# Performance work log

Hardware: AMD Instinct MI355X
Metric: run time of the kernel (lower is better)

Reference implementation:

```python
import jax, jax.numpy as jnp
import numpy as np
import math

NUM_HEADS = 32
NUM_KV_HEADS = 8
HEAD_DIM = 128
ROPE_THETA = 10000.0


def _rope_cos_sin(position_ids, head_dim, dtype):
    # inv_freq: [head_dim/2]
    inv_freq = 1.0 / (ROPE_THETA ** (jnp.arange(0, head_dim, 2, dtype=jnp.float32) / head_dim))
    # freqs: [B, S, head_dim/2]
    freqs = position_ids.astype(jnp.float32)[:, :, None] * inv_freq[None, None, :]
    emb = jnp.concatenate([freqs, freqs], axis=-1)  # [B, S, head_dim]
    return jnp.cos(emb).astype(dtype), jnp.sin(emb).astype(dtype)


def _rotate_half(x):
    h = x.shape[-1] // 2
    return jnp.concatenate([-x[..., h:], x[..., :h]], axis=-1)


def setup_inputs() -> dict:
    key = jax.random.key(0)
    ks = jax.random.split(key, 5)
    B, S, H = 1, 2048, 4096
    kv_dim = NUM_KV_HEADS * HEAD_DIM
    return {
        "hidden_states": jax.random.normal(ks[0], (B, S, H), dtype=jnp.float32),
        "position_ids": jnp.arange(S, dtype=jnp.int64 if jax.config.jax_enable_x64 else jnp.int32)[None, :].repeat(B, axis=0),
        "Wq": jax.random.normal(ks[1], (H, H), dtype=jnp.float32) * 0.02,
        "Wk": jax.random.normal(ks[2], (kv_dim, H), dtype=jnp.float32) * 0.02,
        "Wv": jax.random.normal(ks[3], (kv_dim, H), dtype=jnp.float32) * 0.02,
        "Wo": jax.random.normal(ks[4], (H, H), dtype=jnp.float32) * 0.02,
    }


def reference(hidden_states, position_ids, Wq, Wk, Wv, Wo):
    B, S, H = hidden_states.shape
    groups = NUM_HEADS // NUM_KV_HEADS

    # QKV projections (nn.Linear: x @ W.T, no bias)
    q = (hidden_states @ Wq.T).reshape(B, S, NUM_HEADS, HEAD_DIM).transpose(0, 2, 1, 3)
    k = (hidden_states @ Wk.T).reshape(B, S, NUM_KV_HEADS, HEAD_DIM).transpose(0, 2, 1, 3)
    v = (hidden_states @ Wv.T).reshape(B, S, NUM_KV_HEADS, HEAD_DIM).transpose(0, 2, 1, 3)

    # RoPE
    cos, sin = _rope_cos_sin(position_ids, HEAD_DIM, q.dtype)
    cos = cos[:, None, :, :]  # [B,1,S,hd]
    sin = sin[:, None, :, :]
    q = q * cos + _rotate_half(q) * sin
    k = k * cos + _rotate_half(k) * sin

    # repeat_kv: expand KV heads to match Q heads
    k = jnp.repeat(k, groups, axis=1)  # [B, NUM_HEADS, S, hd]
    v = jnp.repeat(v, groups, axis=1)

    # scores + causal mask + fp32 softmax
    scores = jnp.einsum("bhqd,bhkd->bhqk", q, k) / math.sqrt(HEAD_DIM)
    causal = jnp.tril(jnp.ones((S, S), dtype=bool))
    scores = jnp.where(causal[None, None, :, :], scores, jnp.finfo(jnp.float32).min)
    attn = jax.nn.softmax(scores.astype(jnp.float32), axis=-1).astype(q.dtype)

    # attention output + output projection
    out = jnp.einsum("bhqk,bhkd->bhqd", attn, v)
    out = out.transpose(0, 2, 1, 3).reshape(B, S, H)
    return out @ Wo.T
```

## Files before the change

kernel.cpp:

```cpp
#include <hip/hip_runtime.h>
#include <stdint.h>


typedef __attribute__((ext_vector_type(8))) __bf16 bf16x8;
typedef __attribute__((ext_vector_type(4))) float floatx4;

#define S_LEN 2048
#define HID   4096
#define NH    32
#define NKV   8
#define HD    128

__device__ __forceinline__ unsigned short f2bf(float f) {
  union { float f; uint32_t u; } v; v.f = f;
  return (unsigned short)((v.u + 0x7fffu + ((v.u >> 16) & 1u)) >> 16);
}

__device__ __forceinline__ void gload_lds16(const unsigned short* g, unsigned short* l) {
  __builtin_amdgcn_global_load_lds(
      (const __attribute__((address_space(1))) void*)g,
      (__attribute__((address_space(3))) void*)l,
      16, 0, 0);
}

__global__ void cast_bf16_kernel(const float* __restrict__ in,
                                 unsigned short* __restrict__ out, int n4) {
  int i = blockIdx.x * blockDim.x + threadIdx.x;
  if (i >= n4) return;
  float4 f = ((const float4*)in)[i];
  ushort4 o = make_ushort4(f2bf(f.x), f2bf(f.y), f2bf(f.z), f2bf(f.w));
  ((ushort4*)out)[i] = o;
}

#define BM 128
#define BN 128
#define BK 32

__global__ __launch_bounds__(256) void gemm_bt_kernel(
    const unsigned short* __restrict__ A,
    const unsigned short* __restrict__ B,
    float* __restrict__ C, int M, int N, int K) {
  __shared__ unsigned short As[BM * BK];
  __shared__ unsigned short Bs[BN * BK];
  const int m0 = blockIdx.y * BM;
  const int n0 = blockIdx.x * BN;
  const int tid = threadIdx.x;
  const int lane = tid & 63;
  const int l15 = lane & 15;
  const int quad = lane >> 4;
  const int w = tid >> 6;
  const int wm = (w >> 1) * 64;
  const int wn = (w & 1) * 64;

  floatx4 acc[4][4];
#pragma unroll
  for (int i = 0; i < 4; i++)
#pragma unroll
    for (int j = 0; j < 4; j++) acc[i][j] = (floatx4){0.f, 0.f, 0.f, 0.f};

  const int c0 = tid, c1 = tid + 256;
  const int r0 = c0 >> 2, o0 = (c0 & 3) * 8;
  const int r1 = c1 >> 2, o1 = (c1 & 3) * 8;

  for (int k0 = 0; k0 < K; k0 += BK) {
    __syncthreads();
    gload_lds16(A + (size_t)(m0 + r0) * K + k0 + o0, As + c0 * 8);
    gload_lds16(A + (size_t)(m0 + r1) * K + k0 + o1, As + c1 * 8);
    gload_lds16(B + (size_t)(n0 + r0) * K + k0 + o0, Bs + c0 * 8);
    gload_lds16(B + (size_t)(n0 + r1) * K + k0 + o1, Bs + c1 * 8);
    __syncthreads();

    bf16x8 a_frag[4], b_frag[4];
#pragma unroll
    for (int mt = 0; mt < 4; mt++)
      a_frag[mt] = *(const bf16x8*)&As[(wm + mt * 16 + l15) * BK + quad * 8];
#pragma unroll
    for (int nt = 0; nt < 4; nt++)
      b_frag[nt] = *(const bf16x8*)&Bs[(wn + nt * 16 + l15) * BK + quad * 8];
#pragma unroll
    for (int mt = 0; mt < 4; mt++)
#pragma unroll
      for (int nt = 0; nt < 4; nt++)
        acc[mt][nt] = __builtin_amdgcn_mfma_f32_16x16x32_bf16(
            a_frag[mt], b_frag[nt], acc[mt][nt], 0, 0, 0);
  }

#pragma unroll
  for (int mt = 0; mt < 4; mt++) {
#pragma unroll
    for (int nt = 0; nt < 4; nt++) {
      const int row = m0 + wm + mt * 16 + quad * 4;
      const int col = n0 + wn + nt * 16 + l15;
#pragma unroll
      for (int r = 0; r < 4; r++)
        C[(size_t)(row + r) * N + col] = acc[mt][nt][r];
    }
  }
}

__global__ void rope_kernel(const float* __restrict__ Cqkv,
                            const int* __restrict__ pos_ids,
                            unsigned short* __restrict__ Qb,
                            unsigned short* __restrict__ Kb) {
  int t = blockIdx.x * blockDim.x + threadIdx.x;
  int j = t & 63;
  int s = t >> 6;
  int hh = blockIdx.y;
  float pos = (float)pos_ids[s];
  float ang = pos * exp2f(-0.20762050593045222f * (float)j);
  float c = cosf(ang), sn = sinf(ang);
  if (hh < NH) {
    const float* row = Cqkv + (size_t)s * 6144 + hh * HD;
    float x1 = row[j], x2 = row[j + 64];
    unsigned short* q = Qb + ((size_t)hh * S_LEN + s) * HD;
    q[j]      = f2bf(x1 * c - x2 * sn);
    q[j + 64] = f2bf(x2 * c + x1 * sn);
  } else {
    int kh = hh - NH;
    const float* row = Cqkv + (size_t)s * 6144 + HID + kh * HD;
    float x1 = row[j], x2 = row[j + 64];
    unsigned short* k = Kb + ((size_t)kh * S_LEN + s) * HD;
    k[j]      = f2bf(x1 * c - x2 * sn);
    k[j + 64] = f2bf(x2 * c + x1 * sn);
  }
}

__global__ void vtrans_kernel(const float* __restrict__ Cqkv,
                              unsigned short* __restrict__ Vt) {
  int t = blockIdx.x * blockDim.x + threadIdx.x;
  int s = t & (S_LEN - 1);
  int d = (t >> 11) & (HD - 1);
  int kh = t >> 18;
  Vt[((size_t)kh * HD + d) * S_LEN + s] =
      f2bf(Cqkv[(size_t)s * 6144 + (HID + NKV * HD) + kh * HD + d]);
}

__global__ __launch_bounds__(256, 2) void flash_attn_kernel(
    const unsigned short* __restrict__ Qb, const unsigned short* __restrict__ Kb,
    const unsigned short* __restrict__ Vt, unsigned short* __restrict__ O) {
  __shared__ unsigned short Ks[2][64 * 128];
  __shared__ unsigned short Vs[2][128 * 64];
  __shared__ unsigned short Ps[4][2][16 * 64];
  const int qb = gridDim.x - 1 - blockIdx.x;
  const int q0 = qb * 128;
  const int h = blockIdx.y;
  const int kvh = h >> 2;
  const int tid = threadIdx.x;
  const int lane = tid & 63;
  const int w = tid >> 6;
  const int l15 = lane & 15;
  const int quad = lane >> 4;
  const int qlo = q0 + w * 32;

  const unsigned short* Qh = Qb + (size_t)h * S_LEN * HD;
  const unsigned short* Kh = Kb + (size_t)kvh * S_LEN * HD;
  const unsigned short* Vh = Vt + (size_t)kvh * HD * S_LEN;

  const int kr_[4] = {(tid) >> 4, (tid + 256) >> 4, (tid + 512) >> 4, (tid + 768) >> 4};
  const int nkt = q0 / 64 + 2;

#pragma unroll
  for (int it = 0; it < 4; it++) {
    int c = tid + it * 256;
    int kr = c >> 4, kj = (c & 15) ^ (kr & 15);
    gload_lds16(Kh + (size_t)kr * HD + kj * 8, Ks[0] + c * 8);
    int vd = c >> 3, vj = (c & 7) ^ (vd & 7);
    gload_lds16(Vh + (size_t)vd * S_LEN + vj * 8, Vs[0] + c * 8);
  }

  bf16x8 q_frag[2][4];
#pragma unroll
  for (int mf = 0; mf < 2; mf++)
#pragma unroll
    for (int kk = 0; kk < 4; kk++)
      q_frag[mf][kk] = *(const bf16x8*)&Qh[(size_t)(qlo + mf * 16 + l15) * HD + kk * 32 + quad * 8];

  bf16x8 ones_frag;
  {
    union { unsigned short u; __bf16 b; } ov;
    ov.u = (l15 == 0) ? 0x3F80 : 0;
#pragma unroll
    for (int j = 0; j < 8; j++) ones_frag[j] = ov.b;
  }

  floatx4 o_acc[2][8];
  floatx4 o_l[2];
#pragma unroll
  for (int mf = 0; mf < 2; mf++) {
#pragma unroll
    for (int i = 0; i < 8; i++) o_acc[mf][i] = (floatx4){0.f, 0.f, 0.f, 0.f};
    o_l[mf] = (floatx4){0.f, 0.f, 0.f, 0.f};
  }
  const float SC2 = 0.12751738f;

  for (int kt = 0; kt < nkt; kt++) {
    const int kbase = kt * 64;
    const int buf = kt & 1;
    __syncthreads();

    if (kt + 1 < nkt) {
      const int kb2 = kbase + 64;
#pragma unroll
      for (int it = 0; it < 4; it++) {
        int c = tid + it * 256;
        int kr = c >> 4, kj = (c & 15) ^ (kr & 15);
        gload_lds16(Kh + (size_t)(kb2 + kr) * HD + kj * 8, Ks[buf ^ 1] + c * 8);
        int vd = c >> 3, vj = (c & 7) ^ (vd & 7);
        gload_lds16(Vh + (size_t)vd * S_LEN + kb2 + vj * 8, Vs[buf ^ 1] + c * 8);
      }
    }

    if (kbase <= qlo + 31) {
      floatx4 s_acc[2][4];
#pragma unroll
      for (int mf = 0; mf < 2; mf++)
#pragma unroll
        for (int nt = 0; nt < 4; nt++) s_acc[mf][nt] = (floatx4){0.f, 0.f, 0.f, 0.f};
#pragma unroll
      for (int kk = 0; kk < 4; kk++)
#pragma unroll
        for (int nt = 0; nt < 4; nt++) {
          bf16x8 k_frag = *(const bf16x8*)&Ks[buf][(nt * 16 + l15) * 128 + (((kk * 4 + quad) ^ l15) * 8)];
#pragma unroll
          for (int mf = 0; mf < 2; mf++)
            s_acc[mf][nt] = __builtin_amdgcn_mfma_f32_16x16x32_bf16(
                q_frag[mf][kk], k_frag, s_acc[mf][nt], 0, 0, 0);
        }

      const bool diag = (kbase + 63 > qlo);
#pragma unroll
      for (int mf = 0; mf < 2; mf++) {
#pragma unroll
        for (int nt = 0; nt < 4; nt++) {
          int kc = kbase + nt * 16 + l15;
          int qrow = qlo + mf * 16 + quad * 4;
          int chunk2 = nt * 2 + (l15 >> 3);
          int coff = l15 & 7;
#pragma unroll
          for (int r = 0; r < 4; r++) {
            float pv = exp2f(s_acc[mf][nt][r] * SC2);
            if (diag && kc > qrow + r) pv = 0.f;
            int row = quad * 4 + r;
            Ps[w][mf][row * 64 + ((chunk2 ^ (row & 7)) * 8) + coff] = f2bf(pv);
          }
        }
      }

#pragma unroll
      for (int kk2 = 0; kk2 < 2; kk2++) {
        bf16x8 p_frag[2];
#pragma unroll
        for (int mf = 0; mf < 2; mf++)
          p_frag[mf] = *(const bf16x8*)&Ps[w][mf][l15 * 64 + (((kk2 * 4 + quad) ^ (l15 & 7)) * 8)];
#pragma unroll
        for (int dt = 0; dt < 8; dt++) {
          bf16x8 v_frag = *(const bf16x8*)&Vs[buf][(dt * 16 + l15) * 64 + (((kk2 * 4 + quad) ^ (l15 & 7)) * 8)];
#pragma unroll
          for (int mf = 0; mf < 2; mf++)
            o_acc[mf][dt] = __builtin_amdgcn_mfma_f32_16x16x32_bf16(
                p_frag[mf], v_frag, o_acc[mf][dt], 0, 0, 0);
        }
#pragma unroll
        for (int mf = 0; mf < 2; mf++)
          o_l[mf] = __builtin_amdgcn_mfma_f32_16x16x32_bf16(
              p_frag[mf], ones_frag, o_l[mf], 0, 0, 0);
      }
    }
  }

#pragma unroll
  for (int mf = 0; mf < 2; mf++)
#pragma unroll
    for (int r = 0; r < 4; r++) {
      float lsum = __shfl(o_l[mf][r], lane & 48, 64);
      float inv = 1.f / lsum;
      int qr = qlo + mf * 16 + quad * 4 + r;
#pragma unroll
      for (int dt = 0; dt < 8; dt++)
        O[(size_t)qr * HID + h * HD + dt * 16 + l15] = f2bf(o_acc[mf][dt][r] * inv);
    }
}

extern "C" void kernel_launch(void* const* d_in, const int* in_sizes, int n_in,
                              void* d_out, int out_size, void* d_ws, size_t ws_size,
                              hipStream_t stream) {
  const float* hidden = (const float*)d_in[0];
  const int*   pos    = (const int*)d_in[1];
  const float* Wq     = (const float*)d_in[2];
  const float* Wk     = (const float*)d_in[3];
  const float* Wv     = (const float*)d_in[4];
  const float* Wo     = (const float*)d_in[5];

  char* ws = (char*)d_ws;
  size_t off = 0;
  unsigned short* h_b    = (unsigned short*)(ws + off); off += (size_t)S_LEN * HID * 2;
  unsigned short* Wqkv_b = (unsigned short*)(ws + off); off += (size_t)6144 * HID * 2;
  unsigned short* Wo_b   = (unsigned short*)(ws + off); off += (size_t)HID * HID * 2;
  float*          Cqkv   = (float*)(ws + off);          off += (size_t)S_LEN * 6144 * 4;
  unsigned short* Qb     = (unsigned short*)(ws + off); off += (size_t)NH * S_LEN * HD * 2;
  unsigned short* Kb     = (unsigned short*)(ws + off); off += (size_t)NKV * S_LEN * HD * 2;
  unsigned short* Vt     = (unsigned short*)(ws + off); off += (size_t)NKV * HD * S_LEN * 2;
  unsigned short* attn_b = (unsigned short*)Cqkv;

  cast_bf16_kernel<<<(S_LEN * HID / 4) / 256, 256, 0, stream>>>(hidden, h_b, S_LEN * HID / 4);
  cast_bf16_kernel<<<(HID * HID / 4) / 256, 256, 0, stream>>>(Wq, Wqkv_b, HID * HID / 4);
  cast_bf16_kernel<<<(1024 * HID / 4) / 256, 256, 0, stream>>>(Wk, Wqkv_b + (size_t)4096 * HID, 1024 * HID / 4);
  cast_bf16_kernel<<<(1024 * HID / 4) / 256, 256, 0, stream>>>(Wv, Wqkv_b + (size_t)5120 * HID, 1024 * HID / 4);
  cast_bf16_kernel<<<(HID * HID / 4) / 256, 256, 0, stream>>>(Wo, Wo_b, HID * HID / 4);

  gemm_bt_kernel<<<dim3(6144 / BN, S_LEN / BM), 256, 0, stream>>>(h_b, Wqkv_b, Cqkv, S_LEN, 6144, HID);

  rope_kernel<<<dim3(S_LEN * 64 / 256, NH + NKV), 256, 0, stream>>>(Cqkv, pos, Qb, Kb);
  vtrans_kernel<<<(NKV * HD * S_LEN) / 256, 256, 0, stream>>>(Cqkv, Vt);

  flash_attn_kernel<<<dim3(S_LEN / 128, NH), 256, 0, stream>>>(Qb, Kb, Vt, attn_b);

  gemm_bt_kernel<<<dim3(HID / BN, S_LEN / BM), 256, 0, stream>>>(attn_b, Wo_b, (float*)d_out, S_LEN, HID, HID);
}
```

Baseline: 592.2 us.

## Replace GEMM with 256x256 tile, 4-stage LDS pipeline and swizzled layout

```diff
diff --git a/kernel.cpp b/kernel.cpp
--- a/kernel.cpp
+++ b/kernel.cpp
@@ -32,68 +32,123 @@
   ((ushort4*)out)[i] = o;
 }
 
-#define BM 128
-#define BN 128
-#define BK 32
-
-__global__ __launch_bounds__(256) void gemm_bt_kernel(
+#define GT 32
+
+__global__ __launch_bounds__(512, 2) void gemm_bt256_kernel(
     const unsigned short* __restrict__ A,
     const unsigned short* __restrict__ B,
     float* __restrict__ C, int M, int N, int K) {
-  __shared__ unsigned short As[BM * BK];
-  __shared__ unsigned short Bs[BN * BK];
-  const int m0 = blockIdx.y * BM;
-  const int n0 = blockIdx.x * BN;
+  __shared__ unsigned short As[4][256 * GT];
+  __shared__ unsigned short Bs[4][256 * GT];
+  const int m0 = blockIdx.y * 256;
+  const int n0 = blockIdx.x * 256;
   const int tid = threadIdx.x;
   const int lane = tid & 63;
+  const int wv = tid >> 6;
+  const int wr = wv >> 2;
+  const int wc = wv & 3;
   const int l15 = lane & 15;
   const int quad = lane >> 4;
-  const int w = tid >> 6;
-  const int wm = (w >> 1) * 64;
-  const int wn = (w & 1) * 64;
-
-  floatx4 acc[4][4];
-#pragma unroll
-  for (int i = 0; i < 4; i++)
+
+  const int ch0 = wv * 64 + lane;
+  const int ch1 = ch0 + 512;
+  const int cs0 = ch0 ^ ((ch0 >> 4) & 3);
+  const int cs1 = ch1 ^ ((ch1 >> 4) & 3);
+  const int r0s = cs0 >> 2, c0s = (cs0 & 3) * 8;
+  const int r1s = cs1 >> 2, c1s = (cs1 & 3) * 8;
+
+  floatx4 acc[8][4];
+#pragma unroll
+  for (int i = 0; i < 8; i++)
 #pragma unroll
     for (int j = 0; j < 4; j++) acc[i][j] = (floatx4){0.f, 0.f, 0.f, 0.f};
 
-  const int c0 = tid, c1 = tid + 256;
-  const int r0 = c0 >> 2, o0 = (c0 & 3) * 8;
-  const int r1 = c1 >> 2, o1 = (c1 & 3) * 8;
-
-  for (int k0 = 0; k0 < K; k0 += BK) {
-    __syncthreads();
-    gload_lds16(A + (size_t)(m0 + r0) * K + k0 + o0, As + c0 * 8);
-    gload_lds16(A + (size_t)(m0 + r1) * K + k0 + o1, As + c1 * 8);
-    gload_lds16(B + (size_t)(n0 + r0) * K + k0 + o0, Bs + c0 * 8);
-    gload_lds16(B + (size_t)(n0 + r1) * K + k0 + o1, Bs + c1 * 8);
-    __syncthreads();
-
-    bf16x8 a_frag[4], b_frag[4];
-#pragma unroll
-    for (int mt = 0; mt < 4; mt++)
-      a_frag[mt] = *(const bf16x8*)&As[(wm + mt * 16 + l15) * BK + quad * 8];
-#pragma unroll
-    for (int nt = 0; nt < 4; nt++)
-      b_frag[nt] = *(const bf16x8*)&Bs[(wn + nt * 16 + l15) * BK + quad * 8];
-#pragma unroll
-    for (int mt = 0; mt < 4; mt++)
-#pragma unroll
-      for (int nt = 0; nt < 4; nt++)
-        acc[mt][nt] = __builtin_amdgcn_mfma_f32_16x16x32_bf16(
-            a_frag[mt], b_frag[nt], acc[mt][nt], 0, 0, 0);
-  }
-
-#pragma unroll
-  for (int mt = 0; mt < 4; mt++) {
-#pragma unroll
-    for (int nt = 0; nt < 4; nt++) {
-      const int row = m0 + wm + mt * 16 + quad * 4;
-      const int col = n0 + wn + nt * 16 + l15;
-#pragma unroll
-      for (int r = 0; r < 4; r++)
-        C[(size_t)(row + r) * N + col] = acc[mt][nt][r];
+  const int T = K / GT;
+
+#define STAGE_A(kk0, s)                                                        \
+  do {                                                                         \
+    gload_lds16(A + (size_t)(m0 + r0s) * K + (kk0) + c0s, &As[s][ch0 * 8]);    \
+    gload_lds16(A + (size_t)(m0 + r1s) * K + (kk0) + c1s, &As[s][ch1 * 8]);    \
+  } while (0)
+#define STAGE_B(kk0, s)                                                        \
+  do {                                                                         \
+    gload_lds16(B + (size_t)(n0 + r0s) * K + (kk0) + c0s, &Bs[s][ch0 * 8]);    \
+    gload_lds16(B + (size_t)(n0 + r1s) * K + (kk0) + c1s, &Bs[s][ch1 * 8]);    \
+  } while (0)
+
+  STAGE_A(0, 0);  STAGE_B(0, 0);
+  STAGE_A(GT, 1); STAGE_B(GT, 1);
+  STAGE_A(2 * GT, 2); STAGE_B(2 * GT, 2);
+  asm volatile("s_waitcnt vmcnt(8)" ::: "memory");
+  __builtin_amdgcn_s_barrier();
+
+  for (int t = 0; t < T; ++t) {
+    const int s = t & 3;
+    const int sn = (t + 3) & 3;
+    const bool pf = (t + 3 < T);
+    const int kpf = (t + 3) * GT;
+
+    bf16x8 bfr[4], afr[4];
+#pragma unroll
+    for (int ni = 0; ni < 4; ++ni) {
+      const int row = wc * 64 + ni * 16 + l15;
+      bfr[ni] = *(const bf16x8*)&Bs[s][row * GT + (((quad ^ (row >> 2)) & 3) * 8)];
+    }
+#pragma unroll
+    for (int mi = 0; mi < 4; ++mi) {
+      const int row = wr * 128 + mi * 16 + l15;
+      afr[mi] = *(const bf16x8*)&As[s][row * GT + (((quad ^ (row >> 2)) & 3) * 8)];
+    }
+    if (pf) STAGE_A(kpf, sn);
+    __builtin_amdgcn_s_barrier();
+    asm volatile("s_waitcnt lgkmcnt(0)" ::: "memory");
+    __builtin_amdgcn_sched_barrier(0);
+    __builtin_amdgcn_s_setprio(1);
+#pragma unroll
+    for (int mi = 0; mi < 4; ++mi)
+#pragma unroll
+      for (int ni = 0; ni < 4; ++ni)
+        acc[mi][ni] = __builtin_amdgcn_mfma_f32_16x16x32_bf16(
+            afr[mi], bfr[ni], acc[mi][ni], 0, 0, 0);
+    __builtin_amdgcn_s_setprio(0);
+    __builtin_amdgcn_sched_barrier(0);
+    __builtin_amdgcn_s_barrier();
+
+#pragma unroll
+    for (int mi = 0; mi < 4; ++mi) {
+      const int row = wr * 128 + (mi + 4) * 16 + l15;
+      afr[mi] = *(const bf16x8*)&As[s][row * GT + (((quad ^ (row >> 2)) & 3) * 8)];
+    }
+    if (pf) STAGE_B(kpf, sn);
+    __builtin_amdgcn_s_barrier();
+    asm volatile("s_waitcnt lgkmcnt(0)" ::: "memory");
+    __builtin_amdgcn_sched_barrier(0);
+    __builtin_amdgcn_s_setprio(1);
+#pragma unroll
+    for (int mi = 0; mi < 4; ++mi)
+#pragma unroll
+      for (int ni = 0; ni < 4; ++ni)
+        acc[mi + 4][ni] = __builtin_amdgcn_mfma_f32_16x16x32_bf16(
+            afr[mi], bfr[ni], acc[mi + 4][ni], 0, 0, 0);
+    __builtin_amdgcn_s_setprio(0);
+    __builtin_amdgcn_sched_barrier(0);
+    if (t + 3 < T)      { asm volatile("s_waitcnt vmcnt(8)" ::: "memory"); }
+    else if (t + 2 < T) { asm volatile("s_waitcnt vmcnt(4)" ::: "memory"); }
+    else if (t + 1 < T) { asm volatile("s_waitcnt vmcnt(0)" ::: "memory"); }
+    __builtin_amdgcn_s_barrier();
+  }
+#undef STAGE_A
+#undef STAGE_B
+
+#pragma unroll
+  for (int mi = 0; mi < 8; ++mi) {
+    const int row = m0 + wr * 128 + mi * 16 + quad * 4;
+#pragma unroll
+    for (int ni = 0; ni < 4; ++ni) {
+      const int col = n0 + wc * 64 + ni * 16 + l15;
+#pragma unroll
+      for (int r = 0; r < 4; ++r)
+        C[(size_t)(row + r) * N + col] = acc[mi][ni][r];
     }
   }
 }
@@ -156,7 +211,6 @@
   const unsigned short* Kh = Kb + (size_t)kvh * S_LEN * HD;
   const unsigned short* Vh = Vt + (size_t)kvh * HD * S_LEN;
 
-  const int kr_[4] = {(tid) >> 4, (tid + 256) >> 4, (tid + 512) >> 4, (tid + 768) >> 4};
   const int nkt = q0 / 64 + 2;
 
 #pragma unroll
@@ -308,12 +362,12 @@
   cast_bf16_kernel<<<(1024 * HID / 4) / 256, 256, 0, stream>>>(Wv, Wqkv_b + (size_t)5120 * HID, 1024 * HID / 4);
   cast_bf16_kernel<<<(HID * HID / 4) / 256, 256, 0, stream>>>(Wo, Wo_b, HID * HID / 4);
 
-  gemm_bt_kernel<<<dim3(6144 / BN, S_LEN / BM), 256, 0, stream>>>(h_b, Wqkv_b, Cqkv, S_LEN, 6144, HID);
+  gemm_bt256_kernel<<<dim3(6144 / 256, S_LEN / 256), 512, 0, stream>>>(h_b, Wqkv_b, Cqkv, S_LEN, 6144, HID);
 
   rope_kernel<<<dim3(S_LEN * 64 / 256, NH + NKV), 256, 0, stream>>>(Cqkv, pos, Qb, Kb);
   vtrans_kernel<<<(NKV * HD * S_LEN) / 256, 256, 0, stream>>>(Cqkv, Vt);
 
   flash_attn_kernel<<<dim3(S_LEN / 128, NH), 256, 0, stream>>>(Qb, Kb, Vt, attn_b);
 
-  gemm_bt_kernel<<<dim3(HID / BN, S_LEN / BM), 256, 0, stream>>>(attn_b, Wo_b, (float*)d_out, S_LEN, HID, HID);
-}
+  gemm_bt256_kernel<<<dim3(HID / 256, S_LEN / 256), 512, 0, stream>>>(attn_b, Wo_b, (float*)d_out, S_LEN, HID, HID);
+}
```

Result: slower. 618.8 us (+4.5%).
